# Kernel optimization log

Hardware: AMD Instinct MI355X
Metric: run time of the kernel (lower is better)

## Reference

```python
import jax, jax.numpy as jnp
import numpy as np

N_ITER = 3
B, L, U = 32, 120, 640
INPUT_CAPS = 32 * 9 * 12  # 3456
N_CLASSES = 5
FINAL_DIM = 16
N_REL = 25


def squash(x):
    # x: (B, n_caps, dim); squash along dim (axis=2)
    l2 = jnp.sum(x * x, axis=2, keepdims=True)
    return x * (l2 / (1.0 + l2) / jnp.sqrt(l2))


def conv2d(x, w, b, stride):
    out = jax.lax.conv_general_dilated(
        x, w, window_strides=stride, padding='VALID',
        dimension_numbers=('NCHW', 'OIHW', 'NCHW'))
    return out + b[None, :, None, None]


def setup_inputs() -> dict:
    key = jax.random.key(0)
    ks = jax.random.split(key, 10)
    stdv = 1.0 / np.sqrt(INPUT_CAPS)
    return {
        'input': jax.random.normal(ks[0], (B, 1, L, U), jnp.float32),
        'conv1_w': jax.random.normal(ks[1], (256, 1, L // 4, U // 4), jnp.float32) * 0.02,
        'conv1_b': jnp.zeros((256,), jnp.float32),
        'prim_w': jax.random.normal(ks[2], (256, 256, 10, 10), jnp.float32) * 0.02,
        'prim_b': jnp.zeros((256,), jnp.float32),
        'caps_w': jax.random.uniform(ks[3], (INPUT_CAPS, 8, N_CLASSES * FINAL_DIM),
                                     jnp.float32, -stdv, stdv),
        'b_route': jnp.zeros((INPUT_CAPS, N_CLASSES), jnp.float32),
        'pred_w': jax.random.normal(ks[4], (N_REL, FINAL_DIM), jnp.float32) * 0.1,
        'pred_b': jnp.zeros((N_REL,), jnp.float32),
        'eos_w': jax.random.normal(ks[5], (1, FINAL_DIM), jnp.float32) * 0.1,
        'eos_b': jnp.zeros((1,), jnp.float32),
    }


def reference(input, conv1_w, conv1_b, prim_w, prim_b, caps_w, b_route,
              pred_w, pred_b, eos_w, eos_b):
    # conv1 + relu: (B,1,120,640) -> (B,256,91,121)
    x = jax.nn.relu(conv2d(input, conv1_w, conv1_b, (1, 4)))
    # primary caps conv: -> (B,256,9,12)
    out = conv2d(x, prim_w, prim_b, (10, 10))
    n, _, h, w = out.shape
    out = out.reshape(n, 32, 8, h, w)                 # (B,32,8,9,12)
    out = jnp.transpose(out, (0, 1, 3, 4, 2))         # (B,32,9,12,8)
    u = squash(out.reshape(n, -1, 8))                 # (B,3456,8)
    # caps layer prediction: (B,I,8) x (I,8,O*D) -> (B,I,O,D)
    u_predict = jnp.einsum('bic,icj->bij', u, caps_w)
    u_predict = u_predict.reshape(n, INPUT_CAPS, N_CLASSES, FINAL_DIM)
    # agreement routing
    c = jax.nn.softmax(b_route, axis=1)               # (I,O)
    s = jnp.einsum('io,biod->bod', c, u_predict)
    v = squash(s)
    b_batch = jnp.broadcast_to(b_route, (n, INPUT_CAPS, N_CLASSES))
    for _ in range(N_ITER):
        b_batch = b_batch + jnp.einsum('biod,bod->bio', u_predict, v)
        c = jax.nn.softmax(b_batch, axis=-1)          # (B,I,O)
        s = jnp.einsum('bio,biod->bod', c, u_predict)
        v = squash(s)                                 # (B,O,D)
    predict_logits = v @ pred_w.T + pred_b            # (B,O,25)
    eos_logits = v @ eos_w.T + eos_b                  # (B,O,1)
    logits = jnp.concatenate([predict_logits, eos_logits], axis=-1)
    return jax.nn.log_softmax(logits, axis=-1)
```

## Files before the change

kernel.cpp:

```cpp
#include <hip/hip_runtime.h>

typedef __bf16 bf16x8 __attribute__((ext_vector_type(8)));
typedef __bf16 bf16x4 __attribute__((ext_vector_type(4)));
typedef float  f32x4  __attribute__((ext_vector_type(4)));
typedef unsigned int  uint;
typedef unsigned short ushort_t;

static __device__ __forceinline__ ushort_t f2bf(float f) {
    uint u = __float_as_uint(f);
    return (ushort_t)((u + 0x7fffu + ((u >> 16) & 1u)) >> 16);
}


constexpr size_t OFF_W1F = 0;
constexpr size_t SZ_W1F  = (size_t)256 * 4800 * 2;
constexpr size_t OFF_A2  = OFF_W1F + SZ_W1F;
constexpr size_t SZ_A2   = (size_t)256 * 25600 * 2;
constexpr size_t OFF_X   = OFF_A2 + SZ_A2;
constexpr size_t SZ_X    = (size_t)32 * 90 * 120 * 256 * 2;
constexpr size_t OFF_P   = OFF_X + SZ_X;
constexpr size_t SZ_P    = (size_t)4 * 256 * 32 * 112 * 4;
constexpr size_t OFF_UP  = OFF_X;
constexpr size_t WS_NEED = OFF_P + SZ_P;

__global__ void k0_w1(const float* __restrict__ w, ushort_t* __restrict__ o) {
    int t = blockIdx.x * 256 + threadIdx.x;
    int l   = t & 63;
    int q   = t >> 6;
    int kwc = q % 5;
    int ocb = (q / 5) % 16;
    int kh  = q / 80;
    const float* src = w + (size_t)(ocb * 16 + (l & 15)) * 4800 + kh * 160 + kwc * 32 + (l >> 4) * 8;
    float4 f0 = *(const float4*)src;
    float4 f1 = *(const float4*)(src + 4);
    uint4 pk;
    pk.x = (uint)f2bf(f0.x) | ((uint)f2bf(f0.y) << 16);
    pk.y = (uint)f2bf(f0.z) | ((uint)f2bf(f0.w) << 16);
    pk.z = (uint)f2bf(f1.x) | ((uint)f2bf(f1.y) << 16);
    pk.w = (uint)f2bf(f1.z) | ((uint)f2bf(f1.w) << 16);
    *(uint4*)&o[(size_t)t * 8] = pk;
}

__global__ void k0_a2(const float* __restrict__ w, ushort_t* __restrict__ o) {
    __shared__ ushort_t l[25600];
    int oc2 = blockIdx.x;
    const float* src = w + (size_t)oc2 * 25600;
    for (int idx = threadIdx.x; idx < 25600; idx += 256) l[idx] = f2bf(src[idx]);
    __syncthreads();
    ushort_t* dst = o + (size_t)oc2 * 25600;
    for (int idx = threadIdx.x; idx < 25600; idx += 256) {
        int p = idx >> 8, ic = idx & 255;
        dst[idx] = l[ic * 100 + p];
    }
}

__global__ __launch_bounds__(256, 2) void k1_conv1(const float* __restrict__ inp,
                                                   const ushort_t* __restrict__ w1f,
                                                   const float* __restrict__ cb,
                                                   ushort_t* __restrict__ X) {
    __shared__ ushort_t smem[31680];
    ushort_t* brow = smem;
    const int tid = threadIdx.x, lane = tid & 63, wid = tid >> 6;
    const int wm = wid * 64;
    const int h = blockIdx.x, b = blockIdx.y;
    const int l16 = lane & 15, g8 = (lane >> 4) * 8;
    const int bbase = 4 * l16 + g8;
    f32x4 acc[4][8] = {};

    for (int idx = tid; idx < 5280; idx += 256) {
        int r = idx / 176, c = idx % 176;
        uint2 pk; pk.x = 0u; pk.y = 0u;
        if (c < 160) {
            const float* irow = inp + ((size_t)b * 120 + h + r) * 640;
            float4 f = *(const float4*)&irow[c * 4];
            pk.x = (uint)f2bf(f.x) | ((uint)f2bf(f.y) << 16);
            pk.y = (uint)f2bf(f.z) | ((uint)f2bf(f.w) << 16);
        }
        *(uint2*)&brow[r * 704 + c * 4] = pk;
    }
    __syncthreads();

#pragma unroll 1
    for (int kh = 0; kh < 30; ++kh) {
        bf16x8 bc[19];
        const int rb = kh * 704 + bbase;
#pragma unroll
        for (int t = 0; t < 19; ++t) {
            union { bf16x8 v8; bf16x4 v4[2]; } fr;
            fr.v4[0] = *(const bf16x4*)&brow[rb + 32 * t];
            fr.v4[1] = *(const bf16x4*)&brow[rb + 32 * t + 4];
            bc[t] = fr.v8;
        }
#pragma unroll
        for (int kwc = 0; kwc < 5; ++kwc) {
            bf16x8 af[4];
#pragma unroll
            for (int mt = 0; mt < 4; ++mt) {
                int q = (kh * 16 + wid * 4 + mt) * 5 + kwc;
                af[mt] = *(const bf16x8*)&w1f[(size_t)q * 512 + lane * 8];
            }
#pragma unroll
            for (int nt = 0; nt < 8; ++nt)
#pragma unroll
                for (int mt = 0; mt < 4; ++mt)
                    acc[mt][nt] = __builtin_amdgcn_mfma_f32_16x16x32_bf16(af[mt], bc[2 * nt + kwc], acc[mt][nt], 0, 0, 0);
        }
    }

    float cbv[4][4];
#pragma unroll
    for (int mt = 0; mt < 4; ++mt)
#pragma unroll
        for (int r = 0; r < 4; ++r)
            cbv[mt][r] = cb[wm + mt * 16 + (lane >> 4) * 4 + r];
    __syncthreads();
    ushort_t* cs = smem;
#pragma unroll
    for (int nt = 0; nt < 8; ++nt) {
        int wg = nt * 16 + l16;
        if (wg < 120) {
#pragma unroll
            for (int mt = 0; mt < 4; ++mt)
#pragma unroll
                for (int r = 0; r < 4; ++r) {
                    int oc = wm + mt * 16 + (lane >> 4) * 4 + r;
                    float v = acc[mt][nt][r] + cbv[mt][r];
                    v = v > 0.f ? v : 0.f;
                    cs[wg * 264 + oc] = f2bf(v);
                }
        }
    }
    __syncthreads();
    ushort_t* Xbase = X + ((size_t)b * 90 + h) * 120 * 256;
    for (int idx = tid; idx < 3840; idx += 256) {
        int w = idx >> 5, c = (idx & 31) * 8;
        *(uint4*)&Xbase[(size_t)w * 256 + c] = *(const uint4*)&cs[w * 264 + c];
    }
}

__global__ __launch_bounds__(256) void k2_prim(const ushort_t* __restrict__ X,
                                               const ushort_t* __restrict__ A2,
                                               float* __restrict__ P) {
    const int tid = threadIdx.x, lane = tid & 63, wid = tid >> 6;
    const int mi = blockIdx.x, s = blockIdx.y, b = blockIdx.z;
    const int msub = mi * 128 + wid * 32;
    const int l16 = lane & 15, g8 = (lane >> 4) * 8;
    f32x4 acc[2][7] = {};
    size_t aoff[2];
#pragma unroll
    for (int t = 0; t < 2; ++t) aoff[t] = (size_t)(msub + t * 16 + l16) * 25600 + g8;
    size_t noff[7];
#pragma unroll
    for (int nt = 0; nt < 7; ++nt) {
        int n = nt * 16 + l16; n = n < 108 ? n : 107;
        int h2 = n / 12, w2 = n % 12;
        noff[nt] = (((size_t)b * 90 + 10 * h2) * 120 + 10 * w2) * 256 + g8;
    }
#pragma unroll 1
    for (int p = s * 25; p < s * 25 + 25; ++p) {
        int ph = p / 10, pw = p % 10;
        size_t xb = (size_t)(ph * 120 + pw) * 256;
        size_t ab = (size_t)p * 256;
#pragma unroll
        for (int icc = 0; icc < 8; ++icc) {
            bf16x8 af[2], bfr[7];
#pragma unroll
            for (int t = 0; t < 2; ++t)
                af[t] = *(const bf16x8*)&A2[aoff[t] + ab + icc * 32];
#pragma unroll
            for (int nt = 0; nt < 7; ++nt)
                bfr[nt] = *(const bf16x8*)&X[noff[nt] + xb + icc * 32];
#pragma unroll
            for (int t = 0; t < 2; ++t)
#pragma unroll
                for (int nt = 0; nt < 7; ++nt)
                    acc[t][nt] = __builtin_amdgcn_mfma_f32_16x16x32_bf16(af[t], bfr[nt], acc[t][nt], 0, 0, 0);
        }
    }
#pragma unroll
    for (int t = 0; t < 2; ++t)
#pragma unroll
        for (int nt = 0; nt < 7; ++nt)
#pragma unroll
            for (int r = 0; r < 4; ++r) {
                int n   = nt * 16 + l16;
                int oc2 = msub + t * 16 + (lane >> 4) * 4 + r;
                P[(((size_t)s * 256 + oc2) * 32 + b) * 112 + n] = acc[t][nt][r];
            }
}

__global__ __launch_bounds__(256) void k3_caps(const float* __restrict__ P,
                                               const float* __restrict__ prim_b,
                                               const float* __restrict__ caps_w,
                                               float* __restrict__ UP) {
    int t = blockIdx.x * 256 + threadIdx.x;
    int b = t / 3456, i = t % 3456;
    int cap = i / 108, hw = i % 108;
    float ud[8], l2 = 0.f;
#pragma unroll
    for (int d = 0; d < 8; ++d) {
        int oc2 = cap * 8 + d;
        float v = prim_b[oc2];
#pragma unroll
        for (int s = 0; s < 4; ++s)
            v += P[(((size_t)s * 256 + oc2) * 32 + b) * 112 + hw];
        ud[d] = v; l2 += v * v;
    }
    float scale = sqrtf(l2) / (1.f + l2);
#pragma unroll
    for (int d = 0; d < 8; ++d) ud[d] *= scale;
    const float* cw = caps_w + (size_t)i * 640;
    float* up = UP + ((size_t)b * 3456 + i) * 80;
    for (int j = 0; j < 80; j += 4) {
        f32x4 o = {0.f, 0.f, 0.f, 0.f};
#pragma unroll
        for (int d = 0; d < 8; ++d) {
            f32x4 w = *(const f32x4*)&cw[d * 80 + j];
            o += ud[d] * w;
        }
        *(f32x4*)&up[j] = o;
    }
}

__global__ __launch_bounds__(256) void k4_route(const float* __restrict__ UP,
                                                const float* __restrict__ b_route,
                                                const float* __restrict__ pred_w,
                                                const float* __restrict__ pred_b,
                                                const float* __restrict__ eos_w,
                                                const float* __restrict__ eos_b,
                                                float* __restrict__ out) {
    __shared__ float sred[4][80];
    __shared__ __attribute__((aligned(16))) float sv[80];
    __shared__ float sscale[5];
    __shared__ float lg[130];
    __shared__ float lse[5];
    const int tid = threadIdx.x, lane = tid & 63, wid = tid >> 6;
    const int b = blockIdx.x;

    float br[14][5];
#pragma unroll
    for (int q = 0; q < 14; ++q) {
        int i = tid + q * 256;
        if (i < 3456)
#pragma unroll
            for (int o = 0; o < 5; ++o) br[q][o] = b_route[i * 5 + o];
    }

#pragma unroll 1
    for (int it = 0; it <= 3; ++it) {
        f32x4 a4[20];
#pragma unroll
        for (int q = 0; q < 20; ++q) a4[q] = f32x4{0.f, 0.f, 0.f, 0.f};
#pragma unroll 1
        for (int q = 0; q < 14; ++q) {
            int i = tid + q * 256;
            if (i < 3456) {
                const float* up = UP + ((size_t)b * 3456 + i) * 80;
                f32x4 u4[20];
#pragma unroll
                for (int r = 0; r < 20; ++r) u4[r] = *(const f32x4*)&up[r * 4];
                float bo[5];
#pragma unroll
                for (int o = 0; o < 5; ++o) {
                    float bv = br[q][o];
                    if (it > 0) {
                        f32x4 dv = u4[o * 4 + 0] * (*(const f32x4*)&sv[o * 16 + 0])
                                 + u4[o * 4 + 1] * (*(const f32x4*)&sv[o * 16 + 4])
                                 + u4[o * 4 + 2] * (*(const f32x4*)&sv[o * 16 + 8])
                                 + u4[o * 4 + 3] * (*(const f32x4*)&sv[o * 16 + 12]);
                        bv += dv[0] + dv[1] + dv[2] + dv[3];
                        br[q][o] = bv;
                    }
                    bo[o] = bv;
                }
                float m = fmaxf(fmaxf(fmaxf(bo[0], bo[1]), fmaxf(bo[2], bo[3])), bo[4]);
                float e[5], sum = 0.f;
#pragma unroll
                for (int o = 0; o < 5; ++o) { e[o] = __expf(bo[o] - m); sum += e[o]; }
                float inv = 1.f / sum;
#pragma unroll
                for (int o = 0; o < 5; ++o) {
                    float c = e[o] * inv;
#pragma unroll
                    for (int q2 = 0; q2 < 4; ++q2) a4[o * 4 + q2] += c * u4[o * 4 + q2];
                }
            }
        }
#pragma unroll
        for (int off = 32; off >= 1; off >>= 1)
#pragma unroll
            for (int q = 0; q < 20; ++q)
#pragma unroll
                for (int c = 0; c < 4; ++c) a4[q][c] += __shfl_xor(a4[q][c], off, 64);
        if (lane == 0)
#pragma unroll
            for (int q = 0; q < 20; ++q)
#pragma unroll
                for (int c = 0; c < 4; ++c) sred[wid][q * 4 + c] = a4[q][c];
        __syncthreads();
        if (tid < 80) sv[tid] = sred[0][tid] + sred[1][tid] + sred[2][tid] + sred[3][tid];
        __syncthreads();
        if (tid < 5) {
            float l2 = 0.f;
            for (int d = 0; d < 16; ++d) { float x = sv[tid * 16 + d]; l2 += x * x; }
            sscale[tid] = sqrtf(l2) / (1.f + l2);
        }
        __syncthreads();
        if (tid < 80) sv[tid] *= sscale[tid / 16];
        __syncthreads();
    }
    if (tid < 130) {
        int o = tid / 26, j = tid % 26;
        const float* wv = (j < 25) ? &pred_w[j * 16] : &eos_w[0];
        float dot = (j < 25) ? pred_b[j] : eos_b[0];
        for (int d = 0; d < 16; ++d) dot += sv[o * 16 + d] * wv[d];
        lg[tid] = dot;
    }
    __syncthreads();
    if (tid < 5) {
        float m = lg[tid * 26];
        for (int j = 1; j < 26; ++j) m = fmaxf(m, lg[tid * 26 + j]);
        float sum = 0.f;
        for (int j = 0; j < 26; ++j) sum += expf(lg[tid * 26 + j] - m);
        lse[tid] = m + logf(sum);
    }
    __syncthreads();
    if (tid < 130) out[b * 130 + tid] = lg[tid] - lse[tid / 26];
}

extern "C" void kernel_launch(void* const* d_in, const int* in_sizes, int n_in,
                              void* d_out, int out_size, void* d_ws, size_t ws_size,
                              hipStream_t stream) {
    const float* inp    = (const float*)d_in[0];
    const float* w1     = (const float*)d_in[1];
    const float* cb1    = (const float*)d_in[2];
    const float* w2     = (const float*)d_in[3];
    const float* pb2    = (const float*)d_in[4];
    const float* capsw  = (const float*)d_in[5];
    const float* broute = (const float*)d_in[6];
    const float* predw  = (const float*)d_in[7];
    const float* predb  = (const float*)d_in[8];
    const float* eosw   = (const float*)d_in[9];
    const float* eosb   = (const float*)d_in[10];
    float* out = (float*)d_out;
    char* ws = (char*)d_ws;
    if (ws_size < WS_NEED) return;

    ushort_t* w1f = (ushort_t*)(ws + OFF_W1F);
    ushort_t* a2  = (ushort_t*)(ws + OFF_A2);
    ushort_t* X   = (ushort_t*)(ws + OFF_X);
    float*    P   = (float*)(ws + OFF_P);
    float*    UP  = (float*)(ws + OFF_UP);

    k0_w1   <<<dim3(600),      dim3(256), 0, stream>>>(w1, w1f);
    k0_a2   <<<dim3(256),      dim3(256), 0, stream>>>(w2, a2);
    k1_conv1<<<dim3(90, 32),   dim3(256), 0, stream>>>(inp, w1f, cb1, X);
    k2_prim <<<dim3(2, 4, 32), dim3(256), 0, stream>>>(X, a2, P);
    k3_caps <<<dim3(432),      dim3(256), 0, stream>>>(P, pb2, capsw, UP);
    k4_route<<<dim3(32),       dim3(256), 0, stream>>>(UP, broute, predw, predb, eosw, eosb, out);
}
```

Before: 1.228 ms.

## Restructure conv1 with 32x32 MFMA, bf16 predictions, and split routing across blocks

The conv1 kernel now computes two output rows per 512-thread block using 32x32x16 bf16 MFMA tiles, with the weight prepack layout changed to match. The caps-prediction tensor is stored as bf16 instead of fp32, halving its memory traffic. The single 32-block routing kernel is replaced by four 864-block iteration launches plus a finalize kernel, using partial-sum buffers and a stored routing-logit buffer. This spreads the routing work across the GPU instead of 32 blocks, at the cost of extra launches and reduced precision in the predictions.

```diff
diff --git a/kernel.cpp b/kernel.cpp
--- a/kernel.cpp
+++ b/kernel.cpp
@@ -3,12 +3,21 @@
 typedef __bf16 bf16x8 __attribute__((ext_vector_type(8)));
 typedef __bf16 bf16x4 __attribute__((ext_vector_type(4)));
 typedef float  f32x4  __attribute__((ext_vector_type(4)));
+typedef float  f32x16 __attribute__((ext_vector_type(16)));
 typedef unsigned int  uint;
 typedef unsigned short ushort_t;
 
 static __device__ __forceinline__ ushort_t f2bf(float f) {
     uint u = __float_as_uint(f);
     return (ushort_t)((u + 0x7fffu + ((u >> 16) & 1u)) >> 16);
+}
+static __device__ __forceinline__ f32x4 up4(uint2 p) {
+    f32x4 r;
+    r[0] = __uint_as_float(p.x << 16);
+    r[1] = __uint_as_float(p.x & 0xffff0000u);
+    r[2] = __uint_as_float(p.y << 16);
+    r[3] = __uint_as_float(p.y & 0xffff0000u);
+    return r;
 }
 
 
@@ -21,16 +30,19 @@
 constexpr size_t OFF_P   = OFF_X + SZ_X;
 constexpr size_t SZ_P    = (size_t)4 * 256 * 32 * 112 * 4;
 constexpr size_t OFF_UP  = OFF_X;
+constexpr size_t OFF_BB  = OFF_X + (size_t)24 * 1024 * 1024;
+constexpr size_t OFF_S0  = OFF_X + (size_t)28 * 1024 * 1024;
+constexpr size_t OFF_S1  = OFF_X + (size_t)29 * 1024 * 1024;
 constexpr size_t WS_NEED = OFF_P + SZ_P;
 
 __global__ void k0_w1(const float* __restrict__ w, ushort_t* __restrict__ o) {
     int t = blockIdx.x * 256 + threadIdx.x;
-    int l   = t & 63;
-    int q   = t >> 6;
-    int kwc = q % 5;
-    int ocb = (q / 5) % 16;
+    int l  = t & 63;
+    int q  = t >> 6;
+    int kc  = q % 10;
+    int ocb = (q / 10) % 8;
     int kh  = q / 80;
-    const float* src = w + (size_t)(ocb * 16 + (l & 15)) * 4800 + kh * 160 + kwc * 32 + (l >> 4) * 8;
+    const float* src = w + (size_t)(ocb * 32 + (l & 31)) * 4800 + kh * 160 + kc * 16 + (l >> 5) * 8;
     float4 f0 = *(const float4*)src;
     float4 f1 = *(const float4*)(src + 4);
     uint4 pk;
@@ -54,24 +66,25 @@
     }
 }
 
-__global__ __launch_bounds__(256, 2) void k1_conv1(const float* __restrict__ inp,
+__global__ __launch_bounds__(512, 2) void k1_conv1(const float* __restrict__ inp,
                                                    const ushort_t* __restrict__ w1f,
                                                    const float* __restrict__ cb,
                                                    ushort_t* __restrict__ X) {
     __shared__ ushort_t smem[31680];
     ushort_t* brow = smem;
-    const int tid = threadIdx.x, lane = tid & 63, wid = tid >> 6;
-    const int wm = wid * 64;
-    const int h = blockIdx.x, b = blockIdx.y;
-    const int l16 = lane & 15, g8 = (lane >> 4) * 8;
-    const int bbase = 4 * l16 + g8;
-    f32x4 acc[4][8] = {};
-
-    for (int idx = tid; idx < 5280; idx += 256) {
+    const int tid = threadIdx.x, lane = tid & 63;
+    const int wid = tid >> 6;
+    const int hr = wid >> 2, mg = (wid >> 1) & 1, wb = wid & 1;
+    const int hp = blockIdx.x, b = blockIdx.y;
+    const int h0 = hp * 2;
+    const int l32 = lane & 31, hi8 = (lane >> 5) * 8;
+    f32x16 acc[4][2] = {};
+
+    for (int idx = tid; idx < 5456; idx += 512) {
         int r = idx / 176, c = idx % 176;
         uint2 pk; pk.x = 0u; pk.y = 0u;
         if (c < 160) {
-            const float* irow = inp + ((size_t)b * 120 + h + r) * 640;
+            const float* irow = inp + ((size_t)b * 120 + h0 + r) * 640;
             float4 f = *(const float4*)&irow[c * 4];
             pk.x = (uint)f2bf(f.x) | ((uint)f2bf(f.y) << 16);
             pk.y = (uint)f2bf(f.z) | ((uint)f2bf(f.w) << 16);
@@ -80,61 +93,66 @@
     }
     __syncthreads();
 
+    const int bb0 = wb * 256 + 4 * l32 + hi8;
 #pragma unroll 1
     for (int kh = 0; kh < 30; ++kh) {
-        bf16x8 bc[19];
-        const int rb = kh * 704 + bbase;
-#pragma unroll
-        for (int t = 0; t < 19; ++t) {
-            union { bf16x8 v8; bf16x4 v4[2]; } fr;
-            fr.v4[0] = *(const bf16x4*)&brow[rb + 32 * t];
-            fr.v4[1] = *(const bf16x4*)&brow[rb + 32 * t + 4];
-            bc[t] = fr.v8;
-        }
-#pragma unroll
-        for (int kwc = 0; kwc < 5; ++kwc) {
-            bf16x8 af[4];
+        const int rb = (kh + hr) * 704 + bb0;
+        const ushort_t* wbase = w1f + (size_t)((kh * 8 + mg * 4) * 10) * 512 + lane * 8;
+#pragma unroll 2
+        for (int kc = 0; kc < 10; ++kc) {
+            bf16x8 bfr[2];
+#pragma unroll
+            for (int nt = 0; nt < 2; ++nt) {
+                union { bf16x8 v8; bf16x4 v4[2]; } fr;
+                fr.v4[0] = *(const bf16x4*)&brow[rb + nt * 128 + kc * 16];
+                fr.v4[1] = *(const bf16x4*)&brow[rb + nt * 128 + kc * 16 + 4];
+                bfr[nt] = fr.v8;
+            }
 #pragma unroll
             for (int mt = 0; mt < 4; ++mt) {
-                int q = (kh * 16 + wid * 4 + mt) * 5 + kwc;
-                af[mt] = *(const bf16x8*)&w1f[(size_t)q * 512 + lane * 8];
+                bf16x8 af = *(const bf16x8*)&wbase[(size_t)(mt * 10 + kc) * 512];
+#pragma unroll
+                for (int nt = 0; nt < 2; ++nt)
+                    acc[mt][nt] = __builtin_amdgcn_mfma_f32_32x32x16_bf16(af, bfr[nt], acc[mt][nt], 0, 0, 0);
             }
-#pragma unroll
-            for (int nt = 0; nt < 8; ++nt)
-#pragma unroll
-                for (int mt = 0; mt < 4; ++mt)
-                    acc[mt][nt] = __builtin_amdgcn_mfma_f32_16x16x32_bf16(af[mt], bc[2 * nt + kwc], acc[mt][nt], 0, 0, 0);
-        }
-    }
-
-    float cbv[4][4];
+        }
+    }
+
+    const int hi4 = (lane >> 5) * 4;
+    float cbv[4][16];
 #pragma unroll
     for (int mt = 0; mt < 4; ++mt)
 #pragma unroll
-        for (int r = 0; r < 4; ++r)
-            cbv[mt][r] = cb[wm + mt * 16 + (lane >> 4) * 4 + r];
+        for (int r = 0; r < 16; ++r)
+            cbv[mt][r] = cb[mg * 128 + mt * 32 + (r & 3) + 8 * (r >> 2) + hi4];
+
     __syncthreads();
     ushort_t* cs = smem;
-#pragma unroll
-    for (int nt = 0; nt < 8; ++nt) {
-        int wg = nt * 16 + l16;
-        if (wg < 120) {
+#pragma unroll 1
+    for (int pass = 0; pass < 2; ++pass) {
+        if (hr == pass) {
 #pragma unroll
             for (int mt = 0; mt < 4; ++mt)
 #pragma unroll
-                for (int r = 0; r < 4; ++r) {
-                    int oc = wm + mt * 16 + (lane >> 4) * 4 + r;
-                    float v = acc[mt][nt][r] + cbv[mt][r];
-                    v = v > 0.f ? v : 0.f;
-                    cs[wg * 264 + oc] = f2bf(v);
-                }
-        }
-    }
-    __syncthreads();
-    ushort_t* Xbase = X + ((size_t)b * 90 + h) * 120 * 256;
-    for (int idx = tid; idx < 3840; idx += 256) {
-        int w = idx >> 5, c = (idx & 31) * 8;
-        *(uint4*)&Xbase[(size_t)w * 256 + c] = *(const uint4*)&cs[w * 264 + c];
+                for (int nt = 0; nt < 2; ++nt)
+#pragma unroll
+                    for (int r = 0; r < 16; ++r) {
+                        int w = wb * 64 + nt * 32 + l32;
+                        if (w < 120) {
+                            int oc = mg * 128 + mt * 32 + (r & 3) + 8 * (r >> 2) + hi4;
+                            float v = acc[mt][nt][r] + cbv[mt][r];
+                            v = v > 0.f ? v : 0.f;
+                            cs[w * 264 + oc] = f2bf(v);
+                        }
+                    }
+        }
+        __syncthreads();
+        ushort_t* Xrow = X + ((size_t)b * 90 + h0 + pass) * 120 * 256;
+        for (int idx = tid; idx < 3840; idx += 512) {
+            int w = idx >> 5, c = (idx & 31) * 8;
+            *(uint4*)&Xrow[(size_t)w * 256 + c] = *(const uint4*)&cs[w * 264 + c];
+        }
+        __syncthreads();
     }
 }
 
@@ -192,9 +210,9 @@
 __global__ __launch_bounds__(256) void k3_caps(const float* __restrict__ P,
                                                const float* __restrict__ prim_b,
                                                const float* __restrict__ caps_w,
-                                               float* __restrict__ UP) {
+                                               ushort_t* __restrict__ UP) {
     int t = blockIdx.x * 256 + threadIdx.x;
-    int b = t / 3456, i = t % 3456;
+    int b = t & 31, i = t >> 5;
     int cap = i / 108, hw = i % 108;
     float ud[8], l2 = 0.f;
 #pragma unroll
@@ -210,7 +228,7 @@
 #pragma unroll
     for (int d = 0; d < 8; ++d) ud[d] *= scale;
     const float* cw = caps_w + (size_t)i * 640;
-    float* up = UP + ((size_t)b * 3456 + i) * 80;
+    ushort_t* up = UP + ((size_t)b * 3456 + i) * 80;
     for (int j = 0; j < 80; j += 4) {
         f32x4 o = {0.f, 0.f, 0.f, 0.f};
 #pragma unroll
@@ -218,87 +236,31 @@
             f32x4 w = *(const f32x4*)&cw[d * 80 + j];
             o += ud[d] * w;
         }
-        *(f32x4*)&up[j] = o;
-    }
-}
-
-__global__ __launch_bounds__(256) void k4_route(const float* __restrict__ UP,
-                                                const float* __restrict__ b_route,
-                                                const float* __restrict__ pred_w,
-                                                const float* __restrict__ pred_b,
-                                                const float* __restrict__ eos_w,
-                                                const float* __restrict__ eos_b,
-                                                float* __restrict__ out) {
-    __shared__ float sred[4][80];
+        uint2 pk;
+        pk.x = (uint)f2bf(o[0]) | ((uint)f2bf(o[1]) << 16);
+        pk.y = (uint)f2bf(o[2]) | ((uint)f2bf(o[3]) << 16);
+        *(uint2*)&up[j] = pk;
+    }
+}
+
+__global__ __launch_bounds__(128) void k4_iter(const ushort_t* __restrict__ UP,
+                                               const float* __restrict__ b_route,
+                                               float* __restrict__ BB,
+                                               const float* __restrict__ spIn,
+                                               float* __restrict__ spOut,
+                                               int flags) {
     __shared__ __attribute__((aligned(16))) float sv[80];
+    __shared__ float sred[2][80];
     __shared__ float sscale[5];
-    __shared__ float lg[130];
-    __shared__ float lse[5];
-    const int tid = threadIdx.x, lane = tid & 63, wid = tid >> 6;
-    const int b = blockIdx.x;
-
-    float br[14][5];
-#pragma unroll
-    for (int q = 0; q < 14; ++q) {
-        int i = tid + q * 256;
-        if (i < 3456)
-#pragma unroll
-            for (int o = 0; o < 5; ++o) br[q][o] = b_route[i * 5 + o];
-    }
-
-#pragma unroll 1
-    for (int it = 0; it <= 3; ++it) {
-        f32x4 a4[20];
-#pragma unroll
-        for (int q = 0; q < 20; ++q) a4[q] = f32x4{0.f, 0.f, 0.f, 0.f};
-#pragma unroll 1
-        for (int q = 0; q < 14; ++q) {
-            int i = tid + q * 256;
-            if (i < 3456) {
-                const float* up = UP + ((size_t)b * 3456 + i) * 80;
-                f32x4 u4[20];
-#pragma unroll
-                for (int r = 0; r < 20; ++r) u4[r] = *(const f32x4*)&up[r * 4];
-                float bo[5];
-#pragma unroll
-                for (int o = 0; o < 5; ++o) {
-                    float bv = br[q][o];
-                    if (it > 0) {
-                        f32x4 dv = u4[o * 4 + 0] * (*(const f32x4*)&sv[o * 16 + 0])
-                                 + u4[o * 4 + 1] * (*(const f32x4*)&sv[o * 16 + 4])
-                                 + u4[o * 4 + 2] * (*(const f32x4*)&sv[o * 16 + 8])
-                                 + u4[o * 4 + 3] * (*(const f32x4*)&sv[o * 16 + 12]);
-                        bv += dv[0] + dv[1] + dv[2] + dv[3];
-                        br[q][o] = bv;
-                    }
-                    bo[o] = bv;
-                }
-                float m = fmaxf(fmaxf(fmaxf(bo[0], bo[1]), fmaxf(bo[2], bo[3])), bo[4]);
-                float e[5], sum = 0.f;
-#pragma unroll
-                for (int o = 0; o < 5; ++o) { e[o] = __expf(bo[o] - m); sum += e[o]; }
-                float inv = 1.f / sum;
-#pragma unroll
-                for (int o = 0; o < 5; ++o) {
-                    float c = e[o] * inv;
-#pragma unroll
-                    for (int q2 = 0; q2 < 4; ++q2) a4[o * 4 + q2] += c * u4[o * 4 + q2];
-                }
-            }
-        }
-#pragma unroll
-        for (int off = 32; off >= 1; off >>= 1)
-#pragma unroll
-            for (int q = 0; q < 20; ++q)
-#pragma unroll
-                for (int c = 0; c < 4; ++c) a4[q][c] += __shfl_xor(a4[q][c], off, 64);
-        if (lane == 0)
-#pragma unroll
-            for (int q = 0; q < 20; ++q)
-#pragma unroll
-                for (int c = 0; c < 4; ++c) sred[wid][q * 4 + c] = a4[q][c];
-        __syncthreads();
-        if (tid < 80) sv[tid] = sred[0][tid] + sred[1][tid] + sred[2][tid] + sred[3][tid];
+    const int tid = threadIdx.x, lane = tid & 63, wv = tid >> 6;
+    const int chunk = blockIdx.x, b = blockIdx.y;
+
+    if (flags & 1) {
+        if (tid < 80) {
+            float s = 0.f;
+            for (int c2 = 0; c2 < 27; ++c2) s += spIn[((size_t)b * 27 + c2) * 80 + tid];
+            sv[tid] = s;
+        }
         __syncthreads();
         if (tid < 5) {
             float l2 = 0.f;
@@ -307,8 +269,81 @@
         }
         __syncthreads();
         if (tid < 80) sv[tid] *= sscale[tid / 16];
-        __syncthreads();
-    }
+    }
+    __syncthreads();
+
+    const int i = chunk * 128 + tid;
+    const ushort_t* up = UP + ((size_t)b * 3456 + i) * 80;
+    f32x4 u4[20];
+#pragma unroll
+    for (int r = 0; r < 20; ++r) u4[r] = up4(*(const uint2*)&up[r * 4]);
+
+    float bo[5];
+#pragma unroll
+    for (int o = 0; o < 5; ++o) {
+        float bv = (flags & 2) ? BB[((size_t)b * 3456 + i) * 5 + o] : b_route[i * 5 + o];
+        if (flags & 1) {
+            f32x4 dv = u4[o * 4 + 0] * (*(const f32x4*)&sv[o * 16 + 0])
+                     + u4[o * 4 + 1] * (*(const f32x4*)&sv[o * 16 + 4])
+                     + u4[o * 4 + 2] * (*(const f32x4*)&sv[o * 16 + 8])
+                     + u4[o * 4 + 3] * (*(const f32x4*)&sv[o * 16 + 12]);
+            bv += dv[0] + dv[1] + dv[2] + dv[3];
+        }
+        if (flags & 4) BB[((size_t)b * 3456 + i) * 5 + o] = bv;
+        bo[o] = bv;
+    }
+    float m = fmaxf(fmaxf(fmaxf(bo[0], bo[1]), fmaxf(bo[2], bo[3])), bo[4]);
+    float e[5], sum = 0.f;
+#pragma unroll
+    for (int o = 0; o < 5; ++o) { e[o] = __expf(bo[o] - m); sum += e[o]; }
+    float inv = 1.f / sum;
+    f32x4 a4[20];
+#pragma unroll
+    for (int o = 0; o < 5; ++o) {
+        float c = e[o] * inv;
+#pragma unroll
+        for (int q = 0; q < 4; ++q) a4[o * 4 + q] = c * u4[o * 4 + q];
+    }
+#pragma unroll
+    for (int off = 32; off >= 1; off >>= 1)
+#pragma unroll
+        for (int q = 0; q < 20; ++q)
+#pragma unroll
+            for (int c = 0; c < 4; ++c) a4[q][c] += __shfl_xor(a4[q][c], off, 64);
+    if (lane == 0)
+#pragma unroll
+        for (int q = 0; q < 20; ++q)
+#pragma unroll
+            for (int c = 0; c < 4; ++c) sred[wv][q * 4 + c] = a4[q][c];
+    __syncthreads();
+    if (tid < 80) spOut[((size_t)b * 27 + chunk) * 80 + tid] = sred[0][tid] + sred[1][tid];
+}
+
+__global__ __launch_bounds__(192) void k4_fin(const float* __restrict__ spIn,
+                                              const float* __restrict__ pred_w,
+                                              const float* __restrict__ pred_b,
+                                              const float* __restrict__ eos_w,
+                                              const float* __restrict__ eos_b,
+                                              float* __restrict__ out) {
+    __shared__ __attribute__((aligned(16))) float sv[80];
+    __shared__ float sscale[5];
+    __shared__ float lg[130];
+    __shared__ float lse[5];
+    const int tid = threadIdx.x, b = blockIdx.x;
+    if (tid < 80) {
+        float s = 0.f;
+        for (int c2 = 0; c2 < 27; ++c2) s += spIn[((size_t)b * 27 + c2) * 80 + tid];
+        sv[tid] = s;
+    }
+    __syncthreads();
+    if (tid < 5) {
+        float l2 = 0.f;
+        for (int d = 0; d < 16; ++d) { float x = sv[tid * 16 + d]; l2 += x * x; }
+        sscale[tid] = sqrtf(l2) / (1.f + l2);
+    }
+    __syncthreads();
+    if (tid < 80) sv[tid] *= sscale[tid / 16];
+    __syncthreads();
     if (tid < 130) {
         int o = tid / 26, j = tid % 26;
         const float* wv = (j < 25) ? &pred_w[j * 16] : &eos_w[0];
@@ -350,12 +385,19 @@
     ushort_t* a2  = (ushort_t*)(ws + OFF_A2);
     ushort_t* X   = (ushort_t*)(ws + OFF_X);
     float*    P   = (float*)(ws + OFF_P);
-    float*    UP  = (float*)(ws + OFF_UP);
+    ushort_t* UP  = (ushort_t*)(ws + OFF_UP);
+    float*    BB  = (float*)(ws + OFF_BB);
+    float*    S0  = (float*)(ws + OFF_S0);
+    float*    S1  = (float*)(ws + OFF_S1);
 
     k0_w1   <<<dim3(600),      dim3(256), 0, stream>>>(w1, w1f);
     k0_a2   <<<dim3(256),      dim3(256), 0, stream>>>(w2, a2);
-    k1_conv1<<<dim3(90, 32),   dim3(256), 0, stream>>>(inp, w1f, cb1, X);
+    k1_conv1<<<dim3(45, 32),   dim3(512), 0, stream>>>(inp, w1f, cb1, X);
     k2_prim <<<dim3(2, 4, 32), dim3(256), 0, stream>>>(X, a2, P);
     k3_caps <<<dim3(432),      dim3(256), 0, stream>>>(P, pb2, capsw, UP);
-    k4_route<<<dim3(32),       dim3(256), 0, stream>>>(UP, broute, predw, predb, eosw, eosb, out);
-}
+    k4_iter <<<dim3(27, 32),   dim3(128), 0, stream>>>(UP, broute, BB, S1, S0, 0);
+    k4_iter <<<dim3(27, 32),   dim3(128), 0, stream>>>(UP, broute, BB, S0, S1, 1 | 4);
+    k4_iter <<<dim3(27, 32),   dim3(128), 0, stream>>>(UP, broute, BB, S1, S0, 1 | 2 | 4);
+    k4_iter <<<dim3(27, 32),   dim3(128), 0, stream>>>(UP, broute, BB, S0, S1, 1 | 2);
+    k4_fin  <<<dim3(32),       dim3(192), 0, stream>>>(S1, predw, predb, eosw, eosb, out);
+}
```

Result: slower. 2.488 ms (+102.5%).
